# Performance work log

Measured on AMD Instinct MI355X. Metric: run time of the kernel, lower is better.

The kernel has to match this reference:

```python
import jax, jax.numpy as jnp
import numpy as np

N_BINS = 10
A_CONST = 0.4
C_CONST = 500.0


def entropy(v, n=N_BINS):
    # Faithful to the torch loop: p_i = mean(v >= lo + i*s and v < lo + (i+1)*s),
    # entropy -= p*log(p) for p != 0. Vectorized over the n bins.
    v = v.reshape(-1)
    lo = v.min()
    hi = v.max()
    scale = (hi - lo) / n
    idx = jnp.arange(n, dtype=v.dtype)
    lower = lo + idx * scale                    # [n]
    upper = lower + scale                       # [n]
    mask = (v[None, :] >= lower[:, None]) & (v[None, :] < upper[:, None])  # [n, len(v)]
    p = mask.sum(axis=1).astype(v.dtype) / v.shape[0]
    safe_p = jnp.where(p > 0, p, 1.0)
    return -jnp.sum(jnp.where(p > 0, p * jnp.log(safe_p), 0.0))


def unite(p_i, p_j, w_assess, b_assess):
    # w_local = sigmoid(Linear(|p_i - p_j|)); w_global scalar from entropy gap.
    w_local = jax.nn.sigmoid(jnp.abs(p_i - p_j) @ w_assess.T + b_assess)
    w_global = A_CONST / jnp.pi * jnp.arctan(C_CONST * (entropy(p_i) - entropy(p_j))) + 0.5
    w = w_global * w_local + (1.0 - w_global)
    return p_i * w + p_j * (1.0 - w)


def setup_inputs() -> dict:
    key = jax.random.key(0)
    ks = jax.random.split(key, 11)
    B, S, H, L = 64, 512, 1024, 3
    s = 1.0 / np.sqrt(H)
    return {
        "x": jax.random.normal(ks[0], (B, S, H), jnp.float32),
        "base_dense_w": jax.random.normal(ks[1], (H, H), jnp.float32) * s,
        "base_dense_b": jax.random.normal(ks[2], (H,), jnp.float32) * s,
        "base_out_w": jax.random.normal(ks[3], (L, H), jnp.float32) * s,
        "base_out_b": jax.random.normal(ks[4], (L,), jnp.float32) * s,
        "graft_dense_w": jax.random.normal(ks[5], (H, H), jnp.float32) * s,
        "graft_out_w": jax.random.normal(ks[6], (L, H), jnp.float32) * s,
        "dense_assess_w": jax.random.normal(ks[7], (H, H), jnp.float32) * s,
        "dense_assess_b": jax.random.normal(ks[8], (H,), jnp.float32) * s,
        "out_assess_w": jax.random.normal(ks[9], (H, H), jnp.float32) * s,
        "out_assess_b": jax.random.normal(ks[10], (H,), jnp.float32) * s,
    }


def reference(x, base_dense_w, base_dense_b, base_out_w, base_out_b,
              graft_dense_w, graft_out_w,
              dense_assess_w, dense_assess_b, out_assess_w, out_assess_b):
    # roberta branch; dropout is identity (eval mode)
    h = x[:, 0, :]  # [B, H] CLS token
    # layer 0: dense
    pu0 = unite(base_dense_w, graft_dense_w, dense_assess_w, dense_assess_b)
    h = jnp.tanh(h @ pu0.T + base_dense_b)
    # layer 1: out_proj (final -> return)
    pu1 = unite(base_out_w, graft_out_w, out_assess_w, out_assess_b)
    return h @ pu1.T + base_out_b
```

## Files before the change

### kernel.cpp

```cpp
#include <hip/hip_runtime.h>
#include <hip/hip_bf16.h>
#include <math.h>


#define NBINS 10
typedef short bf8v __attribute__((ext_vector_type(8)));
typedef float f32x4 __attribute__((ext_vector_type(4)));

#define AST(p, v) __hip_atomic_store((p), (v), __ATOMIC_RELAXED, __HIP_MEMORY_SCOPE_AGENT)
#define ALD(p)    __hip_atomic_load((p), __ATOMIC_RELAXED, __HIP_MEMORY_SCOPE_AGENT)

static __device__ __forceinline__ unsigned short f2bf(float f) {
    __hip_bfloat16 h = __float2bfloat16(f);
    return __builtin_bit_cast(unsigned short, h);
}

#define GL2LDS(gp, lp) __builtin_amdgcn_global_load_lds(                       \
    (__attribute__((address_space(1))) void*)(gp),                             \
    (__attribute__((address_space(3))) void*)(lp), 16, 0, 0)

static __device__ __forceinline__ void stage_tile(const unsigned short* __restrict__ src,
                                                  short* lds_tile, int t, int row0, int k0) {
    int r = t >> 2, s = t & 3;
    int kg = s ^ ((r >> 1) & 3);
    GL2LDS(src + (size_t)(row0 + r) * 1024 + k0 + kg * 8, lds_tile + t * 8);
}

static __device__ __forceinline__ int frag_off(int row, int k8) {
    return row * 4 + (k8 ^ ((row >> 1) & 3));
}

static __device__ __forceinline__ float ent_bins(const unsigned* bins, float N) {
    float s = 0.0f;
    for (int b = 0; b < NBINS; b++) {
        float p = __fdiv_rn((float)ALD(&bins[b]), N);
        if (p > 0.0f) s += p * logf(p);
    }
    return -s;
}

__global__ __launch_bounds__(256) void k_prep(
    const float* __restrict__ x, const float* __restrict__ bdw, const float* __restrict__ bow,
    const float* __restrict__ gdw, const float* __restrict__ gow, const float* __restrict__ daw,
    const float* __restrict__ oaw, char* __restrict__ ws) {
    const int blk = blockIdx.x, t = threadIdx.x;
    const int lane = t & 63, wid = t >> 6;
    float* ws_f = (float*)ws;
    unsigned* ws_u = (unsigned*)ws;
    float* slots = ws_f + 320;
    float* S1    = ws_f + 1344;
    unsigned short* Db  = (unsigned short*)(ws + 4227072);
    unsigned short* Wb  = (unsigned short*)(ws + 6324224);
    unsigned short* x0b = (unsigned short*)(ws + 8421376);
    __shared__ float sp[256];
    __shared__ float s_small[16];

    if (blk < 256) {
        float lo0 = INFINITY, hi0 = -INFINITY, lo1 = INFINITY, hi1 = -INFINITY;
        int fbase = blk * 1024 + t;
#pragma unroll
        for (int q = 0; q < 4; q++) {
            int idx = fbase + q * 256;
            float4 a = ((const float4*)bdw)[idx];
            float4 b = ((const float4*)gdw)[idx];
            float4 w = ((const float4*)daw)[idx];
            lo0 = fminf(lo0, fminf(fminf(a.x, a.y), fminf(a.z, a.w)));
            hi0 = fmaxf(hi0, fmaxf(fmaxf(a.x, a.y), fmaxf(a.z, a.w)));
            lo1 = fminf(lo1, fminf(fminf(b.x, b.y), fminf(b.z, b.w)));
            hi1 = fmaxf(hi1, fmaxf(fmaxf(b.x, b.y), fmaxf(b.z, b.w)));
            ushort4 d, ww;
            d.x = f2bf(fabsf(a.x - b.x)); d.y = f2bf(fabsf(a.y - b.y));
            d.z = f2bf(fabsf(a.z - b.z)); d.w = f2bf(fabsf(a.w - b.w));
            ww.x = f2bf(w.x); ww.y = f2bf(w.y); ww.z = f2bf(w.z); ww.w = f2bf(w.w);
            ((ushort4*)Db)[idx] = d;
            ((ushort4*)Wb)[idx] = ww;
        }
        for (int off = 32; off; off >>= 1) {
            lo0 = fminf(lo0, __shfl_down(lo0, off));
            hi0 = fmaxf(hi0, __shfl_down(hi0, off));
            lo1 = fminf(lo1, __shfl_down(lo1, off));
            hi1 = fmaxf(hi1, __shfl_down(hi1, off));
        }
        if (lane == 0) { s_small[wid] = lo0; s_small[4 + wid] = hi0; s_small[8 + wid] = lo1; s_small[12 + wid] = hi1; }
        __syncthreads();
        if (t == 0) {
            slots[blk]       = fminf(fminf(s_small[0], s_small[1]), fminf(s_small[2], s_small[3]));
            slots[256 + blk] = fmaxf(fmaxf(s_small[4], s_small[5]), fmaxf(s_small[6], s_small[7]));
            slots[512 + blk] = fminf(fminf(s_small[8], s_small[9]), fminf(s_small[10], s_small[11]));
            slots[768 + blk] = fmaxf(fmaxf(s_small[12], s_small[13]), fmaxf(s_small[14], s_small[15]));
        }
    } else {
        const int blk2 = blk - 256;
        {
            int d = t >> 4, kq = t & 15;
            if (d < 12) {
                int r = d >> 2, c = blk2 * 4 + (d & 3);
                const float4* bo4 = (const float4*)(bow + r * 1024);
                const float4* go4 = (const float4*)(gow + r * 1024);
                const float4* oa4 = (const float4*)(oaw + c * 1024);
                float s = 0.f;
#pragma unroll
                for (int k4 = kq * 16; k4 < kq * 16 + 16; ++k4) {
                    float4 bv = bo4[k4], gv = go4[k4], wv = oa4[k4];
                    s += fabsf(bv.x - gv.x) * wv.x + fabsf(bv.y - gv.y) * wv.y +
                         fabsf(bv.z - gv.z) * wv.z + fabsf(bv.w - gv.w) * wv.w;
                }
                sp[t] = s;
            }
            __syncthreads();
            if (t < 12) {
                float s = 0.f;
#pragma unroll
                for (int q = 0; q < 16; q++) s += sp[t * 16 + q];
                S1[(t >> 2) * 1024 + blk2 * 4 + (t & 3)] = s;
            }
        }
        if (blk == 256 || blk == 257) {
            const float* p = (blk == 256) ? bow : gow;
            float lo = INFINITY, hi = -INFINITY;
#pragma unroll
            for (int q = 0; q < 12; q++) { float v = p[q * 256 + t]; lo = fminf(lo, v); hi = fmaxf(hi, v); }
            for (int off = 32; off; off >>= 1) { lo = fminf(lo, __shfl_down(lo, off)); hi = fmaxf(hi, __shfl_down(hi, off)); }
            __syncthreads();
            if (lane == 0) { s_small[wid] = lo; s_small[4 + wid] = hi; }
            __syncthreads();
            if (t == 0) {
                ws_f[8 + 2 * (blk - 256)] = fminf(fminf(s_small[0], s_small[1]), fminf(s_small[2], s_small[3]));
                ws_f[9 + 2 * (blk - 256)] = fmaxf(fmaxf(s_small[4], s_small[5]), fmaxf(s_small[6], s_small[7]));
            }
        }
        if (blk == 258) {
            ws_u[64 + t] = 0u;
            if (t < 40) ws_u[16 + t] = 0u;
        }
        if (blk >= 260 && blk < 324) {
            int row = blk - 260;
            float4 v = ((const float4*)(x + (size_t)row * 524288))[t];
            ushort4 o; o.x = f2bf(v.x); o.y = f2bf(v.y); o.z = f2bf(v.z); o.w = f2bf(v.w);
            ((ushort4*)x0b)[row * 256 + t] = o;
        }
    }
}

__global__ __launch_bounds__(256) void k_main(
    const float* __restrict__ bdw, const float* __restrict__ gdw, const float* __restrict__ dab,
    const float* __restrict__ bow, const float* __restrict__ gow, const float* __restrict__ oab,
    char* __restrict__ ws) {
    const int blk = blockIdx.x, t = threadIdx.x;
    const int lane = t & 63, wid = t >> 6;
    const int lr = lane & 15, k8 = lane >> 4;
    const int wr = wid >> 1, wc = wid & 1;

    float* ws_f = (float*)ws;
    unsigned* ws_u = (unsigned*)ws;
    unsigned* bins  = ws_u + 16;
    unsigned* flags = ws_u + 64;
    float* slots = ws_f + 320;
    float* S1    = ws_f + 1344;
    float* pu1   = ws_f + 4480;
    float* part2 = ws_f + 8192;
    const unsigned short* Db  = (const unsigned short*)(ws + 4227072);
    const unsigned short* Wb  = (const unsigned short*)(ws + 6324224);
    const unsigned short* x0b = (const unsigned short*)(ws + 8421376);

    __shared__ short lds_a[2][2048];
    __shared__ short lds_b[2][2048];
    __shared__ short ldsT[64 * 72];
    __shared__ float s_small[16];
    __shared__ unsigned s_hist[NBINS];
    __shared__ float s_wg[2];

    {
        int m, b0, nb;
        if (blk < 120)      { m = 0; b0 = blk;       nb = 120; }
        else if (blk < 240) { m = 1; b0 = blk - 120; nb = 120; }
        else if (blk < 248) { m = 2; b0 = blk - 240; nb = 8; }
        else                { m = 3; b0 = blk - 248; nb = 8; }
        const float* p = (m == 0) ? bdw : (m == 1) ? gdw : (m == 2) ? bow : gow;
        int n = (m < 2) ? 1048576 : 3072;
        float lo, hi;
        if (m < 2) {
            float l = slots[m * 512 + t];
            float h = slots[m * 512 + 256 + t];
            for (int off = 32; off; off >>= 1) { l = fminf(l, __shfl_down(l, off)); h = fmaxf(h, __shfl_down(h, off)); }
            if (lane == 0) { s_small[wid] = l; s_small[4 + wid] = h; }
            __syncthreads();
            lo = fminf(fminf(s_small[0], s_small[1]), fminf(s_small[2], s_small[3]));
            hi = fmaxf(fmaxf(s_small[4], s_small[5]), fmaxf(s_small[6], s_small[7]));
        } else {
            lo = ws_f[8 + 2 * (m - 2)];
            hi = ws_f[9 + 2 * (m - 2)];
        }
        float scale = __fdiv_rn(__fsub_rn(hi, lo), 10.0f);
        float lower[NBINS], upper[NBINS];
#pragma unroll
        for (int b = 0; b < NBINS; b++) {
            lower[b] = __fadd_rn(lo, __fmul_rn((float)b, scale));
            upper[b] = __fadd_rn(lower[b], scale);
        }
        unsigned cn[NBINS] = {};
        for (int i = b0 * 256 + t; i < n; i += nb * 256) {
            float v = p[i];
#pragma unroll
            for (int b = 0; b < NBINS; b++)
                if (v >= lower[b] && v < upper[b]) cn[b]++;
        }
        if (t < NBINS) s_hist[t] = 0;
        __syncthreads();
#pragma unroll
        for (int b = 0; b < NBINS; b++)
            if (cn[b]) atomicAdd(&s_hist[b], cn[b]);
        __syncthreads();
        if (t < NBINS && s_hist[t])
            __hip_atomic_fetch_add(&bins[m * NBINS + t], s_hist[t], __ATOMIC_RELAXED, __HIP_MEMORY_SCOPE_AGENT);
    }
    __syncthreads();
    if (t == 0) AST(&flags[blk], 1u);

    const int bi = ((blk & 7) << 1) | ((blk >> 3) & 1);
    const int bj = blk >> 4;
    f32x4 acc[2][2] = {};
    {
        stage_tile(Db, lds_a[0], t, bi * 64, 0);
        stage_tile(Wb, lds_b[0], t, bj * 64, 0);
        int cur = 0;
        for (int tt = 0; tt < 32; ++tt) {
            __syncthreads();
            if (tt + 1 < 32) {
                stage_tile(Db, lds_a[cur ^ 1], t, bi * 64, (tt + 1) * 32);
                stage_tile(Wb, lds_b[cur ^ 1], t, bj * 64, (tt + 1) * 32);
            }
            const bf8v* Av = (const bf8v*)lds_a[cur];
            const bf8v* Bv = (const bf8v*)lds_b[cur];
            bf8v a0 = Av[frag_off(wr * 32 + lr, k8)];
            bf8v a1 = Av[frag_off(wr * 32 + 16 + lr, k8)];
            bf8v b0 = Bv[frag_off(wc * 32 + lr, k8)];
            bf8v b1 = Bv[frag_off(wc * 32 + 16 + lr, k8)];
            acc[0][0] = __builtin_amdgcn_mfma_f32_16x16x32_bf16(a0, b0, acc[0][0], 0, 0, 0);
            acc[0][1] = __builtin_amdgcn_mfma_f32_16x16x32_bf16(a0, b1, acc[0][1], 0, 0, 0);
            acc[1][0] = __builtin_amdgcn_mfma_f32_16x16x32_bf16(a1, b0, acc[1][0], 0, 0, 0);
            acc[1][1] = __builtin_amdgcn_mfma_f32_16x16x32_bf16(a1, b1, acc[1][1], 0, 0, 0);
            cur ^= 1;
        }
    }

    for (;;) {
        unsigned v = ALD(&flags[t]);
        if (__syncthreads_and((int)(v >= 1u))) break;
        __builtin_amdgcn_s_sleep(1);
    }
    if (t == 0) {
        float e0 = ent_bins(&bins[0], 1048576.0f);
        float e1 = ent_bins(&bins[10], 1048576.0f);
        float e2 = ent_bins(&bins[20], 3072.0f);
        float e3 = ent_bins(&bins[30], 3072.0f);
        const float API = (float)(0.4 / M_PI);
        s_wg[0] = API * atanf(500.0f * (e0 - e1)) + 0.5f;
        s_wg[1] = API * atanf(500.0f * (e2 - e3)) + 0.5f;
    }
    __syncthreads();

    {
        float wg = s_wg[0];
#pragma unroll
        for (int mi = 0; mi < 2; mi++)
#pragma unroll
            for (int mj = 0; mj < 2; mj++)
#pragma unroll
                for (int r = 0; r < 4; r++) {
                    int il = wr * 32 + mi * 16 + k8 * 4 + r;
                    int jl = wc * 32 + mj * 16 + lr;
                    int ig = bi * 64 + il, jg = bj * 64 + jl;
                    float s = acc[mi][mj][r] + dab[jg];
                    float wl = 1.0f / (1.0f + expf(-s));
                    float w = wg * wl + (1.0f - wg);
                    float o = bdw[ig * 1024 + jg] * w + gdw[ig * 1024 + jg] * (1.0f - w);
                    ldsT[il * 72 + jl] = (short)f2bf(o);
                }
        __syncthreads();
        f32x4 ah[2][2] = {};
#pragma unroll
        for (int ks = 0; ks < 2; ks++) {
            bf8v af[2], bf_[2];
#pragma unroll
            for (int mi = 0; mi < 2; mi++) {
                int m = wr * 32 + mi * 16 + lr;
                af[mi] = *(const bf8v*)&x0b[m * 1024 + bj * 64 + ks * 32 + k8 * 8];
            }
#pragma unroll
            for (int mj = 0; mj < 2; mj++) {
                int c = wc * 32 + mj * 16 + lr;
                bf_[mj] = *(const bf8v*)&ldsT[c * 72 + ks * 32 + k8 * 8];
            }
#pragma unroll
            for (int mi = 0; mi < 2; mi++)
#pragma unroll
                for (int mj = 0; mj < 2; mj++)
                    ah[mi][mj] = __builtin_amdgcn_mfma_f32_16x16x32_bf16(af[mi], bf_[mj], ah[mi][mj], 0, 0, 0);
        }
#pragma unroll
        for (int mi = 0; mi < 2; mi++)
#pragma unroll
            for (int mj = 0; mj < 2; mj++)
#pragma unroll
                for (int r = 0; r < 4; r++) {
                    int m = wr * 32 + mi * 16 + k8 * 4 + r;
                    int cg = bi * 64 + wc * 32 + mj * 16 + lr;
                    part2[((size_t)(bj * 64 + m) << 10) + cg] = ah[mi][mj][r];
                }
    }
    if (blk < 16 && t < 192) {
        int r = t >> 6, c = blk * 64 + (t & 63);
        float s1 = S1[r * 1024 + c];
        float wl = 1.0f / (1.0f + expf(-(s1 + oab[c])));
        float wg = s_wg[1];
        float w = wg * wl + (1.0f - wg);
        pu1[r * 1024 + c] = bow[r * 1024 + c] * w + gow[r * 1024 + c] * (1.0f - w);
    }
}

__global__ __launch_bounds__(256) void k_out(
    const float* __restrict__ bdb, const float* __restrict__ bob,
    float* __restrict__ out, const char* __restrict__ ws) {
    const int m = blockIdx.x, t = threadIdx.x;
    const int lane = t & 63, wid = t >> 6;
    const float* ws_f = (const float*)ws;
    const float* pu1   = ws_f + 4480;
    const float* part2 = ws_f + 8192;
    __shared__ float s_small[16];

    const int c0 = t * 4;
    f32x4 s = {0.f, 0.f, 0.f, 0.f};
#pragma unroll
    for (int b = 0; b < 16; b++)
        s += *(const f32x4*)(part2 + ((size_t)(b * 64 + m) << 10) + c0);
    float h0 = tanhf(s[0] + bdb[c0]);
    float h1 = tanhf(s[1] + bdb[c0 + 1]);
    float h2 = tanhf(s[2] + bdb[c0 + 2]);
    float h3 = tanhf(s[3] + bdb[c0 + 3]);
    float p0, p1, p2;
    {
        f32x4 q0 = *(const f32x4*)(pu1 + c0);
        f32x4 q1 = *(const f32x4*)(pu1 + 1024 + c0);
        f32x4 q2 = *(const f32x4*)(pu1 + 2048 + c0);
        p0 = h0 * q0[0] + h1 * q0[1] + h2 * q0[2] + h3 * q0[3];
        p1 = h0 * q1[0] + h1 * q1[1] + h2 * q1[2] + h3 * q1[3];
        p2 = h0 * q2[0] + h1 * q2[1] + h2 * q2[2] + h3 * q2[3];
    }
    for (int off = 32; off; off >>= 1) {
        p0 += __shfl_down(p0, off);
        p1 += __shfl_down(p1, off);
        p2 += __shfl_down(p2, off);
    }
    if (lane == 0) { s_small[wid] = p0; s_small[4 + wid] = p1; s_small[8 + wid] = p2; }
    __syncthreads();
    if (t == 0) {
        out[m * 3 + 0] = s_small[0] + s_small[1] + s_small[2] + s_small[3] + bob[0];
        out[m * 3 + 1] = s_small[4] + s_small[5] + s_small[6] + s_small[7] + bob[1];
        out[m * 3 + 2] = s_small[8] + s_small[9] + s_small[10] + s_small[11] + bob[2];
    }
}

extern "C" void kernel_launch(void* const* d_in, const int* in_sizes, int n_in,
                              void* d_out, int out_size, void* d_ws, size_t ws_size,
                              hipStream_t stream) {
    const float* x   = (const float*)d_in[0];
    const float* bdw = (const float*)d_in[1];
    const float* bdb = (const float*)d_in[2];
    const float* bow = (const float*)d_in[3];
    const float* bob = (const float*)d_in[4];
    const float* gdw = (const float*)d_in[5];
    const float* gow = (const float*)d_in[6];
    const float* daw = (const float*)d_in[7];
    const float* dab = (const float*)d_in[8];
    const float* oaw = (const float*)d_in[9];
    const float* oab = (const float*)d_in[10];
    float* out = (float*)d_out;
    char* ws = (char*)d_ws;

    k_prep<<<512, 256, 0, stream>>>(x, bdw, bow, gdw, gow, daw, oaw, ws);
    k_main<<<256, 256, 0, stream>>>(bdw, gdw, dab, bow, gow, oab, ws);
    k_out<<<64, 256, 0, stream>>>(bdb, bob, out, ws);
}
```

Baseline: 59.20 us.

## Double k_main grid to 512 blocks with 32x64 tiles and 64-wide K steps

Changes the k_main GEMM tiling from 64x64 output tiles with K=32 steps over 256 blocks to 32x64 tiles with K=64 steps over 512 blocks, using a new 8-way XOR swizzle. Histogram work is spread across twice as many blocks, flag space and workspace offsets are moved, and the grid barrier now waits on 512 flags. The intent is to fill more CUs on the MI355X and halve the number of synchronised K iterations. In exchange, each block reads the B tile redundantly across more blocks, and the grid-wide spin barrier now relies on all 512 blocks being co-resident.

```diff
diff --git a/kernel.cpp b/kernel.cpp
--- a/kernel.cpp
+++ b/kernel.cpp
@@ -19,15 +19,13 @@
     (__attribute__((address_space(1))) void*)(gp),                             \
     (__attribute__((address_space(3))) void*)(lp), 16, 0, 0)
 
-static __device__ __forceinline__ void stage_tile(const unsigned short* __restrict__ src,
-                                                  short* lds_tile, int t, int row0, int k0) {
-    int r = t >> 2, s = t & 3;
-    int kg = s ^ ((r >> 1) & 3);
-    GL2LDS(src + (size_t)(row0 + r) * 1024 + k0 + kg * 8, lds_tile + t * 8);
-}
-
-static __device__ __forceinline__ int frag_off(int row, int k8) {
-    return row * 4 + (k8 ^ ((row >> 1) & 3));
+static __device__ __forceinline__ void stage_slot(const unsigned short* __restrict__ src,
+                                                  short* dst, int s, int row0, int k0) {
+    int r = s >> 3, g = (s & 7) ^ (r & 7);
+    GL2LDS(src + (size_t)(row0 + r) * 1024 + k0 + g * 8, dst + s * 8);
+}
+static __device__ __forceinline__ bf8v fr(const short* lds, int row, int G) {
+    return ((const bf8v*)lds)[row * 8 + (G ^ (row & 7))];
 }
 
 static __device__ __forceinline__ float ent_bins(const unsigned* bins, float N) {
@@ -47,8 +45,8 @@
     const int lane = t & 63, wid = t >> 6;
     float* ws_f = (float*)ws;
     unsigned* ws_u = (unsigned*)ws;
-    float* slots = ws_f + 320;
-    float* S1    = ws_f + 1344;
+    float* slots = ws_f + 576;
+    float* S1    = ws_f + 1600;
     unsigned short* Db  = (unsigned short*)(ws + 4227072);
     unsigned short* Wb  = (unsigned short*)(ws + 6324224);
     unsigned short* x0b = (unsigned short*)(ws + 8421376);
@@ -131,6 +129,7 @@
         }
         if (blk == 258) {
             ws_u[64 + t] = 0u;
+            ws_u[320 + t] = 0u;
             if (t < 40) ws_u[16 + t] = 0u;
         }
         if (blk >= 260 && blk < 324) {
@@ -155,27 +154,27 @@
     unsigned* ws_u = (unsigned*)ws;
     unsigned* bins  = ws_u + 16;
     unsigned* flags = ws_u + 64;
-    float* slots = ws_f + 320;
-    float* S1    = ws_f + 1344;
-    float* pu1   = ws_f + 4480;
+    float* slots = ws_f + 576;
+    float* S1    = ws_f + 1600;
+    float* pu1   = ws_f + 4736;
     float* part2 = ws_f + 8192;
     const unsigned short* Db  = (const unsigned short*)(ws + 4227072);
     const unsigned short* Wb  = (const unsigned short*)(ws + 6324224);
     const unsigned short* x0b = (const unsigned short*)(ws + 8421376);
 
     __shared__ short lds_a[2][2048];
-    __shared__ short lds_b[2][2048];
-    __shared__ short ldsT[64 * 72];
+    __shared__ short lds_b[2][4096];
+    __shared__ short ldsT[32 * 72];
     __shared__ float s_small[16];
     __shared__ unsigned s_hist[NBINS];
     __shared__ float s_wg[2];
 
     {
         int m, b0, nb;
-        if (blk < 120)      { m = 0; b0 = blk;       nb = 120; }
-        else if (blk < 240) { m = 1; b0 = blk - 120; nb = 120; }
-        else if (blk < 248) { m = 2; b0 = blk - 240; nb = 8; }
-        else                { m = 3; b0 = blk - 248; nb = 8; }
+        if (blk < 240)      { m = 0; b0 = blk;       nb = 240; }
+        else if (blk < 480) { m = 1; b0 = blk - 240; nb = 240; }
+        else if (blk < 496) { m = 2; b0 = blk - 480; nb = 16; }
+        else                { m = 3; b0 = blk - 496; nb = 16; }
         const float* p = (m == 0) ? bdw : (m == 1) ? gdw : (m == 2) ? bow : gow;
         int n = (m < 2) ? 1048576 : 3072;
         float lo, hi;
@@ -199,6 +198,7 @@
             upper[b] = __fadd_rn(lower[b], scale);
         }
         unsigned cn[NBINS] = {};
+#pragma unroll 4
         for (int i = b0 * 256 + t; i < n; i += nb * 256) {
             float v = p[i];
 #pragma unroll
@@ -217,36 +217,39 @@
     __syncthreads();
     if (t == 0) AST(&flags[blk], 1u);
 
-    const int bi = ((blk & 7) << 1) | ((blk >> 3) & 1);
-    const int bj = blk >> 4;
-    f32x4 acc[2][2] = {};
+    const int c8 = blk & 7, rr = blk >> 3;
+    const int bi = ((c8 >> 1) << 3) | (rr >> 3);
+    const int bj = ((c8 & 1) << 3) | (rr & 7);
+    f32x4 acc0 = {0.f, 0.f, 0.f, 0.f}, acc1 = {0.f, 0.f, 0.f, 0.f};
     {
-        stage_tile(Db, lds_a[0], t, bi * 64, 0);
-        stage_tile(Wb, lds_b[0], t, bj * 64, 0);
+        stage_slot(Db, lds_a[0], t, bi * 32, 0);
+        stage_slot(Wb, lds_b[0], t, bj * 64, 0);
+        stage_slot(Wb, lds_b[0], t + 256, bj * 64, 0);
         int cur = 0;
-        for (int tt = 0; tt < 32; ++tt) {
-            __syncthreads();
-            if (tt + 1 < 32) {
-                stage_tile(Db, lds_a[cur ^ 1], t, bi * 64, (tt + 1) * 32);
-                stage_tile(Wb, lds_b[cur ^ 1], t, bj * 64, (tt + 1) * 32);
-            }
-            const bf8v* Av = (const bf8v*)lds_a[cur];
-            const bf8v* Bv = (const bf8v*)lds_b[cur];
-            bf8v a0 = Av[frag_off(wr * 32 + lr, k8)];
-            bf8v a1 = Av[frag_off(wr * 32 + 16 + lr, k8)];
-            bf8v b0 = Bv[frag_off(wc * 32 + lr, k8)];
-            bf8v b1 = Bv[frag_off(wc * 32 + 16 + lr, k8)];
-            acc[0][0] = __builtin_amdgcn_mfma_f32_16x16x32_bf16(a0, b0, acc[0][0], 0, 0, 0);
-            acc[0][1] = __builtin_amdgcn_mfma_f32_16x16x32_bf16(a0, b1, acc[0][1], 0, 0, 0);
-            acc[1][0] = __builtin_amdgcn_mfma_f32_16x16x32_bf16(a1, b0, acc[1][0], 0, 0, 0);
-            acc[1][1] = __builtin_amdgcn_mfma_f32_16x16x32_bf16(a1, b1, acc[1][1], 0, 0, 0);
+        for (int tt = 0; tt < 16; ++tt) {
+            __syncthreads();
+            if (tt + 1 < 16) {
+                int k0 = (tt + 1) * 64;
+                stage_slot(Db, lds_a[cur ^ 1], t, bi * 32, k0);
+                stage_slot(Wb, lds_b[cur ^ 1], t, bj * 64, k0);
+                stage_slot(Wb, lds_b[cur ^ 1], t + 256, bj * 64, k0);
+            }
+#pragma unroll
+            for (int kk = 0; kk < 2; kk++) {
+                bf8v a  = fr(lds_a[cur], wr * 16 + lr, kk * 4 + k8);
+                bf8v b0 = fr(lds_b[cur], wc * 32 + lr, kk * 4 + k8);
+                bf8v b1 = fr(lds_b[cur], wc * 32 + 16 + lr, kk * 4 + k8);
+                acc0 = __builtin_amdgcn_mfma_f32_16x16x32_bf16(a, b0, acc0, 0, 0, 0);
+                acc1 = __builtin_amdgcn_mfma_f32_16x16x32_bf16(a, b1, acc1, 0, 0, 0);
+            }
             cur ^= 1;
         }
     }
 
     for (;;) {
-        unsigned v = ALD(&flags[t]);
-        if (__syncthreads_and((int)(v >= 1u))) break;
+        unsigned v0 = ALD(&flags[t]);
+        unsigned v1 = ALD(&flags[t + 256]);
+        if (__syncthreads_and((int)(v0 >= 1u && v1 >= 1u))) break;
         __builtin_amdgcn_s_sleep(1);
     }
     if (t == 0) {
@@ -263,51 +266,41 @@
     {
         float wg = s_wg[0];
 #pragma unroll
-        for (int mi = 0; mi < 2; mi++)
-#pragma unroll
-            for (int mj = 0; mj < 2; mj++)
-#pragma unroll
-                for (int r = 0; r < 4; r++) {
-                    int il = wr * 32 + mi * 16 + k8 * 4 + r;
-                    int jl = wc * 32 + mj * 16 + lr;
-                    int ig = bi * 64 + il, jg = bj * 64 + jl;
-                    float s = acc[mi][mj][r] + dab[jg];
-                    float wl = 1.0f / (1.0f + expf(-s));
-                    float w = wg * wl + (1.0f - wg);
-                    float o = bdw[ig * 1024 + jg] * w + gdw[ig * 1024 + jg] * (1.0f - w);
-                    ldsT[il * 72 + jl] = (short)f2bf(o);
-                }
+        for (int j = 0; j < 2; j++) {
+            f32x4 a = j ? acc1 : acc0;
+#pragma unroll
+            for (int r = 0; r < 4; r++) {
+                int il = wr * 16 + k8 * 4 + r;
+                int jl = wc * 32 + j * 16 + lr;
+                int ig = bi * 32 + il, jg = bj * 64 + jl;
+                float s = a[r] + dab[jg];
+                float wl = 1.0f / (1.0f + expf(-s));
+                float w = wg * wl + (1.0f - wg);
+                float o = bdw[ig * 1024 + jg] * w + gdw[ig * 1024 + jg] * (1.0f - w);
+                ldsT[il * 72 + jl] = (short)f2bf(o);
+            }
+        }
         __syncthreads();
-        f32x4 ah[2][2] = {};
+        f32x4 ah0 = {0.f, 0.f, 0.f, 0.f}, ah1 = {0.f, 0.f, 0.f, 0.f};
 #pragma unroll
         for (int ks = 0; ks < 2; ks++) {
-            bf8v af[2], bf_[2];
-#pragma unroll
-            for (int mi = 0; mi < 2; mi++) {
-                int m = wr * 32 + mi * 16 + lr;
-                af[mi] = *(const bf8v*)&x0b[m * 1024 + bj * 64 + ks * 32 + k8 * 8];
-            }
-#pragma unroll
-            for (int mj = 0; mj < 2; mj++) {
-                int c = wc * 32 + mj * 16 + lr;
-                bf_[mj] = *(const bf8v*)&ldsT[c * 72 + ks * 32 + k8 * 8];
-            }
-#pragma unroll
-            for (int mi = 0; mi < 2; mi++)
-#pragma unroll
-                for (int mj = 0; mj < 2; mj++)
-                    ah[mi][mj] = __builtin_amdgcn_mfma_f32_16x16x32_bf16(af[mi], bf_[mj], ah[mi][mj], 0, 0, 0);
-        }
-#pragma unroll
-        for (int mi = 0; mi < 2; mi++)
-#pragma unroll
-            for (int mj = 0; mj < 2; mj++)
-#pragma unroll
-                for (int r = 0; r < 4; r++) {
-                    int m = wr * 32 + mi * 16 + k8 * 4 + r;
-                    int cg = bi * 64 + wc * 32 + mj * 16 + lr;
-                    part2[((size_t)(bj * 64 + m) << 10) + cg] = ah[mi][mj][r];
-                }
+            int cl = wc * 16 + lr;
+            bf8v b = *(const bf8v*)&ldsT[cl * 72 + ks * 32 + k8 * 8];
+            bf8v a0 = *(const bf8v*)&x0b[(wr * 32 + lr) * 1024 + bj * 64 + ks * 32 + k8 * 8];
+            bf8v a1 = *(const bf8v*)&x0b[(wr * 32 + 16 + lr) * 1024 + bj * 64 + ks * 32 + k8 * 8];
+            ah0 = __builtin_amdgcn_mfma_f32_16x16x32_bf16(a0, b, ah0, 0, 0, 0);
+            ah1 = __builtin_amdgcn_mfma_f32_16x16x32_bf16(a1, b, ah1, 0, 0, 0);
+        }
+#pragma unroll
+        for (int mi = 0; mi < 2; mi++) {
+            f32x4 ah = mi ? ah1 : ah0;
+#pragma unroll
+            for (int r = 0; r < 4; r++) {
+                int m = wr * 32 + mi * 16 + k8 * 4 + r;
+                int cg = bi * 32 + wc * 16 + lr;
+                part2[((size_t)(bj * 64 + m) << 10) + cg] = ah[r];
+            }
+        }
     }
     if (blk < 16 && t < 192) {
         int r = t >> 6, c = blk * 64 + (t & 63);
@@ -325,7 +318,7 @@
     const int m = blockIdx.x, t = threadIdx.x;
     const int lane = t & 63, wid = t >> 6;
     const float* ws_f = (const float*)ws;
-    const float* pu1   = ws_f + 4480;
+    const float* pu1   = ws_f + 4736;
     const float* part2 = ws_f + 8192;
     __shared__ float s_small[16];
 
@@ -379,6 +372,6 @@
     char* ws = (char*)d_ws;
 
     k_prep<<<512, 256, 0, stream>>>(x, bdw, bow, gdw, gow, daw, oaw, ws);
-    k_main<<<256, 256, 0, stream>>>(bdw, gdw, dab, bow, gow, oab, ws);
+    k_main<<<512, 256, 0, stream>>>(bdw, gdw, dab, bow, gow, oab, ws);
     k_out<<<64, 256, 0, stream>>>(bdb, bob, out, ws);
 }
```

Result: faster. 55.10 us, median of 2 (-6.9%).
